# Optimization experiments

Measured on AMD Instinct MI355X. Metric: run time of the kernel, lower is better.

Reference implementation:

```python
import jax, jax.numpy as jnp
import numpy as np

HEADS = 16
DIM_HEAD = 64


def setup_inputs() -> dict:
    key = jax.random.key(0)
    ks = jax.random.split(key, 5)
    b, n, dim = 4, 2048, 1024
    return {
        "x": jax.random.normal(ks[0], (b, n, dim), dtype=jnp.float32),
        "Wq": jax.random.normal(ks[1], (dim, HEADS * DIM_HEAD), dtype=jnp.float32) * (dim ** -0.5),
        "Wkv": jax.random.normal(ks[2], (dim, DIM_HEAD), dtype=jnp.float32) * (dim ** -0.5),
        "null_kv": jax.random.normal(ks[3], (DIM_HEAD,), dtype=jnp.float32),
        "Wout": jax.random.normal(ks[4], (HEADS * DIM_HEAD, dim), dtype=jnp.float32) * ((HEADS * DIM_HEAD) ** -0.5),
    }


def reference(x, Wq, Wkv, null_kv, Wout):
    b, n, dim = x.shape
    scale = DIM_HEAD ** -0.5
    # q: [b, h, n, d], pre-scaled
    q = (x @ Wq).reshape(b, n, HEADS, DIM_HEAD).transpose(0, 2, 1, 3) * scale
    # shared single-head kv: [b, n, d], prepend null token -> [b, n+1, d]
    kv = x @ Wkv
    kv = jnp.concatenate([jnp.broadcast_to(null_kv, (b, 1, DIM_HEAD)), kv], axis=1)
    # sim: [b, h, n, n+1]
    sim = jnp.einsum('bhid,bjd->bhij', q, kv)
    mask_value = -jnp.finfo(sim.dtype).max
    # causal: query i may attend kv cols 0..i+1 (null at col 0)
    i, j = sim.shape[-2], sim.shape[-1]
    causal_mask = jnp.triu(jnp.ones((i, j), dtype=bool), k=j - i + 1)
    sim = jnp.where(causal_mask, mask_value, sim)
    attn = jax.nn.softmax(sim.astype(jnp.float32), axis=-1)
    out = jnp.einsum('bhij,bjd->bhid', attn, kv.astype(jnp.float32))
    out = out.transpose(0, 2, 1, 3).reshape(b, n, HEADS * DIM_HEAD)
    return out @ Wout
```

## Files before the change

### kernel.cpp

```cpp
#include <hip/hip_runtime.h>
#include <hip/hip_bf16.h>

#define HEADS  16
#define DHEAD  64
#define BATCH  4
#define SEQ    2048
#define DIM    1024
#define KVROWS 2112
#define CSHIFT 24.0f

typedef __hip_bfloat16 bf16;
typedef __attribute__((ext_vector_type(8))) short s8v;
typedef __attribute__((ext_vector_type(4))) short s4v;
typedef __attribute__((ext_vector_type(4))) float f4v;

__device__ __forceinline__ void gl_lds16(const void* g, void* l) {
  __builtin_amdgcn_global_load_lds(
      (const __attribute__((address_space(1))) unsigned int*)g,
      (__attribute__((address_space(3))) unsigned int*)l, 16, 0, 0);
}

__global__ void convert_kernel(const float* __restrict__ in, bf16* __restrict__ out) {
  const size_t i = ((size_t)blockIdx.x * 256 + threadIdx.x) * 8;
  const float4 a = *(const float4*)&in[i];
  const float4 b = *(const float4*)&in[i + 4];
  bf16 v[8] = {__float2bfloat16(a.x), __float2bfloat16(a.y),
               __float2bfloat16(a.z), __float2bfloat16(a.w),
               __float2bfloat16(b.x), __float2bfloat16(b.y),
               __float2bfloat16(b.z), __float2bfloat16(b.w)};
  *(s8v*)&out[i] = *(s8v*)v;
}

__global__ void transpose_kernel(const float* __restrict__ in, bf16* __restrict__ out,
                                 int R, int C) {
  __shared__ bf16 tile[32][33];
  const int c0 = blockIdx.x * 32, r0 = blockIdx.y * 32;
  const int tx = threadIdx.x, ty = threadIdx.y;
#pragma unroll
  for (int i = 0; i < 32; i += 8)
    tile[ty + i][tx] = __float2bfloat16(in[(size_t)(r0 + ty + i) * C + c0 + tx]);
  __syncthreads();
#pragma unroll
  for (int i = 0; i < 32; i += 8)
    out[(size_t)(c0 + ty + i) * R + r0 + tx] = tile[tx][ty + i];
}

template <typename OT>
__global__ __launch_bounds__(256) void gemm_async_kernel(
    const bf16* __restrict__ A, const bf16* __restrict__ BT,
    OT* __restrict__ C, int K, int c_ld, float alpha) {
  __shared__ bf16 As[128 * 32];
  __shared__ bf16 Bs[128 * 32];
  const int m0 = blockIdx.x * 128, n0 = blockIdx.y * 128;
  const int t = threadIdx.x;
  const int w = t >> 6, l = t & 63, lr = l & 15, lq = l >> 4;
  const int wm = (w & 1) * 64, wn = (w >> 1) * 64;
  f4v acc[4][4] = {};

  const int rowl = l >> 2;
  const int cl = ((l & 3) ^ ((l >> 3) & 3)) * 8;
  const bf16* gA0 = A  + (size_t)(m0 + 32 * w + rowl) * K + cl;
  const bf16* gA1 = A  + (size_t)(m0 + 32 * w + 16 + rowl) * K + cl;
  const bf16* gB0 = BT + (size_t)(n0 + 32 * w + rowl) * K + cl;
  const bf16* gB1 = BT + (size_t)(n0 + 32 * w + 16 + rowl) * K + cl;
  bf16* lA0 = As + (2 * w) * 512;
  bf16* lA1 = As + (2 * w + 1) * 512;
  bf16* lB0 = Bs + (2 * w) * 512;
  bf16* lB1 = Bs + (2 * w + 1) * 512;

  const int sw = lq ^ ((lr >> 1) & 3);
  const s8v* As16 = (const s8v*)As;
  const s8v* Bs16 = (const s8v*)Bs;

  for (int k0 = 0; k0 < K; k0 += 32) {
    __syncthreads();
    gl_lds16(gA0 + k0, lA0);
    gl_lds16(gA1 + k0, lA1);
    gl_lds16(gB0 + k0, lB0);
    gl_lds16(gB1 + k0, lB1);
    __syncthreads();
    s8v a[4], b[4];
#pragma unroll
    for (int mt = 0; mt < 4; mt++) a[mt] = As16[(wm + mt * 16 + lr) * 4 + sw];
#pragma unroll
    for (int ct = 0; ct < 4; ct++) b[ct] = Bs16[(wn + ct * 16 + lr) * 4 + sw];
#pragma unroll
    for (int mt = 0; mt < 4; mt++)
#pragma unroll
      for (int ct = 0; ct < 4; ct++)
        acc[mt][ct] = __builtin_amdgcn_mfma_f32_16x16x32_bf16(a[mt], b[ct], acc[mt][ct], 0, 0, 0);
  }
#pragma unroll
  for (int mt = 0; mt < 4; mt++)
#pragma unroll
    for (int ct = 0; ct < 4; ct++)
#pragma unroll
      for (int r = 0; r < 4; r++) {
        const int row = m0 + wm + mt * 16 + lq * 4 + r;
        const int col = n0 + wn + ct * 16 + lr;
        const float v = acc[mt][ct][r] * alpha;
        if constexpr (__is_same(OT, float)) C[(size_t)row * c_ld + col] = v;
        else                                C[(size_t)row * c_ld + col] = __float2bfloat16(v);
      }
}

__global__ __launch_bounds__(256) void gemm_kv_kernel(
    const bf16* __restrict__ A, const bf16* __restrict__ BT,
    bf16* __restrict__ kvbuf, bf16* __restrict__ kvbufT, int K) {
  __shared__ bf16 As[128][32];
  __shared__ bf16 Bs[64][32];
  const int m0 = blockIdx.x * 128;
  const int t = threadIdx.x;
  const int w = t >> 6, l = t & 63, lr = l & 15, lq = l >> 4;
  f4v acc[2][4] = {};
  const int arow = t >> 1, acol = (t & 1) * 16;
  const int brow = t >> 2, bcol = (t & 3) * 8;

  for (int k0 = 0; k0 < K; k0 += 32) {
    __syncthreads();
    *(s8v*)&As[arow][acol]     = *(const s8v*)&A[(size_t)(m0 + arow) * K + k0 + acol];
    *(s8v*)&As[arow][acol + 8] = *(const s8v*)&A[(size_t)(m0 + arow) * K + k0 + acol + 8];
    *(s8v*)&Bs[brow][bcol]     = *(const s8v*)&BT[(size_t)brow * K + k0 + bcol];
    __syncthreads();
    s8v a0 = *(const s8v*)&As[w * 32 + lr][lq * 8];
    s8v a1 = *(const s8v*)&As[w * 32 + 16 + lr][lq * 8];
#pragma unroll
    for (int ct = 0; ct < 4; ct++) {
      s8v bf = *(const s8v*)&Bs[ct * 16 + lr][lq * 8];
      acc[0][ct] = __builtin_amdgcn_mfma_f32_16x16x32_bf16(a0, bf, acc[0][ct], 0, 0, 0);
      acc[1][ct] = __builtin_amdgcn_mfma_f32_16x16x32_bf16(a1, bf, acc[1][ct], 0, 0, 0);
    }
  }
#pragma unroll
  for (int mt = 0; mt < 2; mt++)
#pragma unroll
    for (int ct = 0; ct < 4; ct++)
#pragma unroll
      for (int r = 0; r < 4; r++) {
        const int m = m0 + w * 32 + mt * 16 + lq * 4 + r;
        const int col = ct * 16 + lr;
        const int bb = m >> 11, jj = (m & 2047) + 1;
        const bf16 v = __float2bfloat16(acc[mt][ct][r]);
        kvbuf [(size_t)(bb * KVROWS + jj) * DHEAD + col] = v;
        kvbufT[(size_t)(bb * DHEAD + col) * KVROWS + jj] = v;
      }
}

__global__ void fill_null_tail_kernel(const float* __restrict__ null_kv,
                                      bf16* __restrict__ kvbuf,
                                      bf16* __restrict__ kvbufT) {
  const int idx = blockIdx.x * 256 + threadIdx.x;
  const int d = idx & 63;
  const int s = (idx >> 6) & 63;
  const int b = idx >> 12;
  const int row = (s == 0) ? 0 : 2048 + s;
  const bf16 v = (s == 0) ? __float2bfloat16(null_kv[d]) : __float2bfloat16(0.f);
  kvbuf [(size_t)(b * KVROWS + row) * DHEAD + d] = v;
  kvbufT[(size_t)(b * DHEAD + d) * KVROWS + row] = v;
}

__global__ __launch_bounds__(256) void attn_kernel(
    const bf16* __restrict__ q,
    const bf16* __restrict__ kv,
    const bf16* __restrict__ kvT,
    bf16* __restrict__ o) {
  __shared__ bf16 kvs [64][68];
  __shared__ bf16 kvsT[64][68];
  __shared__ bf16 Ps[4][16][68];
  const int t = threadIdx.x, w = t >> 6, l = t & 63, lr = l & 15, lq = l >> 4;
  const int blk = blockIdx.x;
  const int qt = 31 - (blk >> 5);
  const int rem = blk & 31, hp = rem >> 2, b = rem & 3;
  const int q0 = qt * 64;
  const int iw = q0 + w * 16 + lr;

  const bf16* qbase = q + ((size_t)(b * SEQ) + iw) * DIM + hp * 128;
  s8v qb[2][2];
#pragma unroll
  for (int hh = 0; hh < 2; hh++) {
    qb[hh][0] = *(const s8v*)&qbase[hh * 64 + lq * 8];
    qb[hh][1] = *(const s8v*)&qbase[hh * 64 + 32 + lq * 8];
  }

  f4v oaccT[2][4] = {};
  f4v lacc[2] = {};
  const short onebf = (short)0x3F80;
  const s8v ones = {onebf, onebf, onebf, onebf, onebf, onebf, onebf, onebf};

  const bf16* kvb  = kv  + (size_t)b * KVROWS * DHEAD;
  const bf16* kvTb = kvT + (size_t)b * DHEAD * KVROWS;
  const int jend = q0 + 65;
  const int srow = t >> 2, scol = (t & 3) * 16;

  s8v rkv0 = *(const s8v*)&kvb[(size_t)srow * DHEAD + scol];
  s8v rkv1 = *(const s8v*)&kvb[(size_t)srow * DHEAD + scol + 8];
  s8v rkT0 = *(const s8v*)&kvTb[(size_t)srow * KVROWS + scol];
  s8v rkT1 = *(const s8v*)&kvTb[(size_t)srow * KVROWS + scol + 8];

  for (int j0 = 0; j0 < jend; j0 += 64) {
    __syncthreads();
    *(s8v*)&kvs[srow][scol]      = rkv0;
    *(s8v*)&kvs[srow][scol + 8]  = rkv1;
    *(s8v*)&kvsT[srow][scol]     = rkT0;
    *(s8v*)&kvsT[srow][scol + 8] = rkT1;
    __syncthreads();

    const int jn = min(j0 + 64, KVROWS - 64);
    rkv0 = *(const s8v*)&kvb[(size_t)(jn + srow) * DHEAD + scol];
    rkv1 = *(const s8v*)&kvb[(size_t)(jn + srow) * DHEAD + scol + 8];
    rkT0 = *(const s8v*)&kvTb[(size_t)srow * KVROWS + jn + scol];
    rkT1 = *(const s8v*)&kvTb[(size_t)srow * KVROWS + jn + scol + 8];

    f4v st[2][4];
    __builtin_amdgcn_s_setprio(1);
#pragma unroll
    for (int jt = 0; jt < 4; jt++) {
      s8v a0 = *(const s8v*)&kvs[jt * 16 + lr][lq * 8];
      s8v a1 = *(const s8v*)&kvs[jt * 16 + lr][32 + lq * 8];
#pragma unroll
      for (int hh = 0; hh < 2; hh++) {
        f4v z = {-CSHIFT, -CSHIFT, -CSHIFT, -CSHIFT};
        z = __builtin_amdgcn_mfma_f32_16x16x32_bf16(a0, qb[hh][0], z, 0, 0, 0);
        z = __builtin_amdgcn_mfma_f32_16x16x32_bf16(a1, qb[hh][1], z, 0, 0, 0);
        st[hh][jt] = z;
      }
    }
    __builtin_amdgcn_s_setprio(0);

    const bool diag = (j0 + 62 > q0 + w * 16);
    s8v pb[2][2];
#pragma unroll
    for (int hh = 0; hh < 2; hh++) {
      if (diag) {
#pragma unroll
        for (int jt = 0; jt < 4; jt++)
#pragma unroll
          for (int r = 0; r < 4; r++) {
            const int jg = j0 + jt * 16 + lq * 4 + r;
            if (jg > iw + 1) st[hh][jt][r] = -1e30f;
          }
      }
#pragma unroll
      for (int jt = 0; jt < 4; jt++)
#pragma unroll
        for (int r = 0; r < 4; r++)
          st[hh][jt][r] = exp2f(st[hh][jt][r]);

#pragma unroll
      for (int jt = 0; jt < 4; jt++) {
        s4v pk;
#pragma unroll
        for (int r = 0; r < 4; r++) {
          bf16 h16 = __float2bfloat16(st[hh][jt][r]);
          pk[r] = *(short*)&h16;
        }
        *(s4v*)&Ps[w][lr][jt * 16 + lq * 4] = pk;
      }
      pb[hh][0] = *(const s8v*)&Ps[w][lr][lq * 8];
      pb[hh][1] = *(const s8v*)&Ps[w][lr][32 + lq * 8];
    }

    __builtin_amdgcn_s_setprio(1);
#pragma unroll
    for (int hh = 0; hh < 2; hh++) {
      lacc[hh] = __builtin_amdgcn_mfma_f32_16x16x32_bf16(ones, pb[hh][0], lacc[hh], 0, 0, 0);
      lacc[hh] = __builtin_amdgcn_mfma_f32_16x16x32_bf16(ones, pb[hh][1], lacc[hh], 0, 0, 0);
    }
#pragma unroll
    for (int dt = 0; dt < 4; dt++) {
      s8v a0 = *(const s8v*)&kvsT[dt * 16 + lr][lq * 8];
      s8v a1 = *(const s8v*)&kvsT[dt * 16 + lr][32 + lq * 8];
#pragma unroll
      for (int hh = 0; hh < 2; hh++) {
        oaccT[hh][dt] = __builtin_amdgcn_mfma_f32_16x16x32_bf16(a0, pb[hh][0], oaccT[hh][dt], 0, 0, 0);
        oaccT[hh][dt] = __builtin_amdgcn_mfma_f32_16x16x32_bf16(a1, pb[hh][1], oaccT[hh][dt], 0, 0, 0);
      }
    }
    __builtin_amdgcn_s_setprio(0);
  }

#pragma unroll
  for (int hh = 0; hh < 2; hh++) {
    const float inv = 1.0f / lacc[hh][0];
#pragma unroll
    for (int dt = 0; dt < 4; dt++) {
      s4v pk;
#pragma unroll
      for (int r = 0; r < 4; r++) {
        bf16 h16 = __float2bfloat16(oaccT[hh][dt][r] * inv);
        pk[r] = *(short*)&h16;
      }
      *(s4v*)&Ps[w][lr][dt * 16 + lq * 4] = pk;
    }
    const int orow = l >> 2, od = (l & 3) * 16;
    s8v o0 = *(const s8v*)&Ps[w][orow][od];
    s8v o1 = *(const s8v*)&Ps[w][orow][od + 8];
    bf16* op = o + ((size_t)(b * SEQ) + q0 + w * 16 + orow) * DIM + hp * 128 + hh * 64 + od;
    *(s8v*)&op[0] = o0;
    *(s8v*)&op[8] = o1;
  }
}

extern "C" void kernel_launch(void* const* d_in, const int* in_sizes, int n_in,
                              void* d_out, int out_size, void* d_ws, size_t ws_size,
                              hipStream_t stream) {
  const float* x       = (const float*)d_in[0];
  const float* Wq      = (const float*)d_in[1];
  const float* Wkv     = (const float*)d_in[2];
  const float* null_kv = (const float*)d_in[3];
  const float* Wout    = (const float*)d_in[4];
  float* out = (float*)d_out;

  char* dob = (char*)d_out;
  bf16* q      = (bf16*)dob;
  bf16* kvbufT = (bf16*)(dob + (size_t)16 * 1024 * 1024);
  char* p = (char*)d_ws;
  bf16* att   = (bf16*)p;
  bf16* xb    = (bf16*)(p + (size_t)16 * 1024 * 1024);
  bf16* WoutT = (bf16*)(p + (size_t)32 * 1024 * 1024);
  bf16* kvbuf = (bf16*)(p + (size_t)34 * 1024 * 1024);
  bf16* WqT   = att;
  bf16* WkvT  = att + (size_t)DIM * DIM;

  convert_kernel<<<(BATCH * SEQ * DIM) / (256 * 8), 256, 0, stream>>>(x, xb);

  const dim3 tb(32, 8);
  transpose_kernel<<<dim3(32, 32), tb, 0, stream>>>(Wq,   WqT,   DIM, DIM);
  transpose_kernel<<<dim3(2, 32),  tb, 0, stream>>>(Wkv,  WkvT,  DIM, DHEAD);
  transpose_kernel<<<dim3(32, 32), tb, 0, stream>>>(Wout, WoutT, DIM, DIM);

  gemm_async_kernel<bf16><<<dim3(64, 8), 256, 0, stream>>>(xb, WqT, q, DIM, DIM,
                                                           0.125f * 1.44269504089f);
  gemm_kv_kernel<<<64, 256, 0, stream>>>(xb, WkvT, kvbuf, kvbufT, DIM);
  fill_null_tail_kernel<<<(BATCH * 64 * 64) / 256, 256, 0, stream>>>(null_kv, kvbuf, kvbufT);

  attn_kernel<<<32 * 8 * BATCH, 256, 0, stream>>>(q, kvbuf, kvbufT, att);

  gemm_async_kernel<float><<<dim3(64, 8), 256, 0, stream>>>(att, WoutT, out, DIM, DIM, 1.0f);
}
```

Before: 255.5 us.

## Split long causal attention tiles across two blocks and add combine kernel

Query tiles in the upper half of the sequence now have their KV range split between two blocks, each writing unnormalised bf16 partial outputs and row sums. A new combine kernel adds the two partials and normalises them. This balances the causal workload and raises the block count from 1024 to 1536 to shorten the long tail of the heaviest tiles. The cost is an extra launch, the partial-buffer traffic and the bf16 rounding of unnormalised partials. The setprio hints are also dropped and the PV MFMAs are interleaved per head.

```diff
diff --git a/kernel.cpp b/kernel.cpp
--- a/kernel.cpp
+++ b/kernel.cpp
@@ -163,16 +163,34 @@
     const bf16* __restrict__ q,
     const bf16* __restrict__ kv,
     const bf16* __restrict__ kvT,
-    bf16* __restrict__ o) {
+    bf16* __restrict__ o,
+    bf16* __restrict__ opart,
+    float* __restrict__ lpart) {
   __shared__ bf16 kvs [64][68];
   __shared__ bf16 kvsT[64][68];
   __shared__ bf16 Ps[4][16][68];
   const int t = threadIdx.x, w = t >> 6, l = t & 63, lr = l & 15, lq = l >> 4;
   const int blk = blockIdx.x;
-  const int qt = 31 - (blk >> 5);
-  const int rem = blk & 31, hp = rem >> 2, b = rem & 3;
+  int qt, hp, b, half;
+  bool split;
+  if (blk < 1024) {
+    split = true;
+    qt = 31 - (blk >> 6);
+    const int rem = blk & 63;
+    half = rem >> 5; hp = (rem >> 2) & 7; b = rem & 3;
+  } else {
+    split = false;
+    const int r2 = blk - 1024;
+    qt = 15 - (r2 >> 5);
+    const int rem = r2 & 31;
+    half = 0; hp = rem >> 2; b = rem & 3;
+  }
   const int q0 = qt * 64;
   const int iw = q0 + w * 16 + lr;
+  const int nA    = (qt + 3) >> 1;
+  const int js0   = (split && half) ? nA * 64 : 0;
+  const int jend  = (split && !half) ? nA * 64 : q0 + 65;
+  const int jlast = (jend - 1) & ~63;
 
   const bf16* qbase = q + ((size_t)(b * SEQ) + iw) * DIM + hp * 128;
   s8v qb[2][2];
@@ -189,15 +207,14 @@
 
   const bf16* kvb  = kv  + (size_t)b * KVROWS * DHEAD;
   const bf16* kvTb = kvT + (size_t)b * DHEAD * KVROWS;
-  const int jend = q0 + 65;
   const int srow = t >> 2, scol = (t & 3) * 16;
 
-  s8v rkv0 = *(const s8v*)&kvb[(size_t)srow * DHEAD + scol];
-  s8v rkv1 = *(const s8v*)&kvb[(size_t)srow * DHEAD + scol + 8];
-  s8v rkT0 = *(const s8v*)&kvTb[(size_t)srow * KVROWS + scol];
-  s8v rkT1 = *(const s8v*)&kvTb[(size_t)srow * KVROWS + scol + 8];
-
-  for (int j0 = 0; j0 < jend; j0 += 64) {
+  s8v rkv0 = *(const s8v*)&kvb[(size_t)(js0 + srow) * DHEAD + scol];
+  s8v rkv1 = *(const s8v*)&kvb[(size_t)(js0 + srow) * DHEAD + scol + 8];
+  s8v rkT0 = *(const s8v*)&kvTb[(size_t)srow * KVROWS + js0 + scol];
+  s8v rkT1 = *(const s8v*)&kvTb[(size_t)srow * KVROWS + js0 + scol + 8];
+
+  for (int j0 = js0; j0 < jend; j0 += 64) {
     __syncthreads();
     *(s8v*)&kvs[srow][scol]      = rkv0;
     *(s8v*)&kvs[srow][scol + 8]  = rkv1;
@@ -205,14 +222,13 @@
     *(s8v*)&kvsT[srow][scol + 8] = rkT1;
     __syncthreads();
 
-    const int jn = min(j0 + 64, KVROWS - 64);
+    const int jn = min(j0 + 64, jlast);
     rkv0 = *(const s8v*)&kvb[(size_t)(jn + srow) * DHEAD + scol];
     rkv1 = *(const s8v*)&kvb[(size_t)(jn + srow) * DHEAD + scol + 8];
     rkT0 = *(const s8v*)&kvTb[(size_t)srow * KVROWS + jn + scol];
     rkT1 = *(const s8v*)&kvTb[(size_t)srow * KVROWS + jn + scol + 8];
 
     f4v st[2][4];
-    __builtin_amdgcn_s_setprio(1);
 #pragma unroll
     for (int jt = 0; jt < 4; jt++) {
       s8v a0 = *(const s8v*)&kvs[jt * 16 + lr][lq * 8];
@@ -225,10 +241,8 @@
         st[hh][jt] = z;
       }
     }
-    __builtin_amdgcn_s_setprio(0);
 
     const bool diag = (j0 + 62 > q0 + w * 16);
-    s8v pb[2][2];
 #pragma unroll
     for (int hh = 0; hh < 2; hh++) {
       if (diag) {
@@ -256,38 +270,94 @@
         }
         *(s4v*)&Ps[w][lr][jt * 16 + lq * 4] = pk;
       }
-      pb[hh][0] = *(const s8v*)&Ps[w][lr][lq * 8];
-      pb[hh][1] = *(const s8v*)&Ps[w][lr][32 + lq * 8];
-    }
-
-    __builtin_amdgcn_s_setprio(1);
+      const s8v pb0 = *(const s8v*)&Ps[w][lr][lq * 8];
+      const s8v pb1 = *(const s8v*)&Ps[w][lr][32 + lq * 8];
+
+      lacc[hh] = __builtin_amdgcn_mfma_f32_16x16x32_bf16(ones, pb0, lacc[hh], 0, 0, 0);
+      lacc[hh] = __builtin_amdgcn_mfma_f32_16x16x32_bf16(ones, pb1, lacc[hh], 0, 0, 0);
+
+#pragma unroll
+      for (int dt = 0; dt < 4; dt++) {
+        s8v a0 = *(const s8v*)&kvsT[dt * 16 + lr][lq * 8];
+        s8v a1 = *(const s8v*)&kvsT[dt * 16 + lr][32 + lq * 8];
+        oaccT[hh][dt] = __builtin_amdgcn_mfma_f32_16x16x32_bf16(a0, pb0, oaccT[hh][dt], 0, 0, 0);
+        oaccT[hh][dt] = __builtin_amdgcn_mfma_f32_16x16x32_bf16(a1, pb1, oaccT[hh][dt], 0, 0, 0);
+      }
+    }
+  }
+
+  if (!split) {
 #pragma unroll
     for (int hh = 0; hh < 2; hh++) {
-      lacc[hh] = __builtin_amdgcn_mfma_f32_16x16x32_bf16(ones, pb[hh][0], lacc[hh], 0, 0, 0);
-      lacc[hh] = __builtin_amdgcn_mfma_f32_16x16x32_bf16(ones, pb[hh][1], lacc[hh], 0, 0, 0);
-    }
+      const float inv = 1.0f / lacc[hh][0];
+#pragma unroll
+      for (int dt = 0; dt < 4; dt++) {
+        s4v pk;
+#pragma unroll
+        for (int r = 0; r < 4; r++) {
+          bf16 h16 = __float2bfloat16(oaccT[hh][dt][r] * inv);
+          pk[r] = *(short*)&h16;
+        }
+        *(s4v*)&Ps[w][lr][dt * 16 + lq * 4] = pk;
+      }
+      const int orow = l >> 2, od = (l & 3) * 16;
+      s8v o0 = *(const s8v*)&Ps[w][orow][od];
+      s8v o1 = *(const s8v*)&Ps[w][orow][od + 8];
+      bf16* op = o + ((size_t)(b * SEQ) + q0 + w * 16 + orow) * DIM + hp * 128 + hh * 64 + od;
+      *(s8v*)&op[0] = o0;
+      *(s8v*)&op[8] = o1;
+    }
+  } else {
+    const int comb = ((qt - 16) * 8 + hp) * 4 + b;
+    bf16* ob = opart + ((size_t)(comb * 2 + half)) * 8192;
+#pragma unroll
+    for (int hh = 0; hh < 2; hh++) {
+#pragma unroll
+      for (int dt = 0; dt < 4; dt++) {
+        s4v pk;
+#pragma unroll
+        for (int r = 0; r < 4; r++) {
+          bf16 h16 = __float2bfloat16(oaccT[hh][dt][r]);
+          pk[r] = *(short*)&h16;
+        }
+        *(s4v*)&ob[(size_t)((((w * 2 + hh) * 4 + dt) * 64 + l) * 4)] = pk;
+      }
+      if (lq == 0)
+        lpart[(((size_t)(comb * 2 + half) * 4 + w) * 2 + hh) * 16 + lr] = lacc[hh][0];
+    }
+  }
+}
+
+__global__ __launch_bounds__(256) void combine_kernel(
+    const bf16* __restrict__ opart, const float* __restrict__ lpart,
+    bf16* __restrict__ o) {
+  __shared__ bf16 Ps[4][16][68];
+  const int t = threadIdx.x, w = t >> 6, l = t & 63, lr = l & 15, lq = l >> 4;
+  const int blk = blockIdx.x;
+  const int qs = blk >> 5;
+  const int rem = blk & 31, hp = rem >> 2, b = rem & 3;
+  const int qt = qs + 16, q0 = qt * 64;
+  const int comb = (qs * 8 + hp) * 4 + b;
+  const bf16* oA = opart + (size_t)(comb * 2 + 0) * 8192;
+  const bf16* oB = opart + (size_t)(comb * 2 + 1) * 8192;
+
+#pragma unroll
+  for (int hh = 0; hh < 2; hh++) {
+    const float lA = lpart[(((size_t)(comb * 2 + 0) * 4 + w) * 2 + hh) * 16 + lr];
+    const float lB = lpart[(((size_t)(comb * 2 + 1) * 4 + w) * 2 + hh) * 16 + lr];
+    const float inv = 1.0f / (lA + lB);
 #pragma unroll
     for (int dt = 0; dt < 4; dt++) {
-      s8v a0 = *(const s8v*)&kvsT[dt * 16 + lr][lq * 8];
-      s8v a1 = *(const s8v*)&kvsT[dt * 16 + lr][32 + lq * 8];
-#pragma unroll
-      for (int hh = 0; hh < 2; hh++) {
-        oaccT[hh][dt] = __builtin_amdgcn_mfma_f32_16x16x32_bf16(a0, pb[hh][0], oaccT[hh][dt], 0, 0, 0);
-        oaccT[hh][dt] = __builtin_amdgcn_mfma_f32_16x16x32_bf16(a1, pb[hh][1], oaccT[hh][dt], 0, 0, 0);
-      }
-    }
-    __builtin_amdgcn_s_setprio(0);
-  }
-
-#pragma unroll
-  for (int hh = 0; hh < 2; hh++) {
-    const float inv = 1.0f / lacc[hh][0];
-#pragma unroll
-    for (int dt = 0; dt < 4; dt++) {
+      const size_t off = (size_t)((((w * 2 + hh) * 4 + dt) * 64 + l) * 4);
+      const s4v pa = *(const s4v*)&oA[off];
+      const s4v pc = *(const s4v*)&oB[off];
       s4v pk;
 #pragma unroll
       for (int r = 0; r < 4; r++) {
-        bf16 h16 = __float2bfloat16(oaccT[hh][dt][r] * inv);
+        short sa = pa[r], sc = pc[r];
+        const float va = __bfloat162float(*(bf16*)&sa);
+        const float vc = __bfloat162float(*(bf16*)&sc);
+        bf16 h16 = __float2bfloat16((va + vc) * inv);
         pk[r] = *(short*)&h16;
       }
       *(s4v*)&Ps[w][lr][dt * 16 + lq * 4] = pk;
@@ -314,6 +384,7 @@
   char* dob = (char*)d_out;
   bf16* q      = (bf16*)dob;
   bf16* kvbufT = (bf16*)(dob + (size_t)16 * 1024 * 1024);
+  float* lpart = (float*)(dob + (size_t)18 * 1024 * 1024);
   char* p = (char*)d_ws;
   bf16* att   = (bf16*)p;
   bf16* xb    = (bf16*)(p + (size_t)16 * 1024 * 1024);
@@ -321,6 +392,7 @@
   bf16* kvbuf = (bf16*)(p + (size_t)34 * 1024 * 1024);
   bf16* WqT   = att;
   bf16* WkvT  = att + (size_t)DIM * DIM;
+  bf16* opart = xb;
 
   convert_kernel<<<(BATCH * SEQ * DIM) / (256 * 8), 256, 0, stream>>>(x, xb);
 
@@ -334,7 +406,8 @@
   gemm_kv_kernel<<<64, 256, 0, stream>>>(xb, WkvT, kvbuf, kvbufT, DIM);
   fill_null_tail_kernel<<<(BATCH * 64 * 64) / 256, 256, 0, stream>>>(null_kv, kvbuf, kvbufT);
 
-  attn_kernel<<<32 * 8 * BATCH, 256, 0, stream>>>(q, kvbuf, kvbufT, att);
+  attn_kernel<<<1536, 256, 0, stream>>>(q, kvbuf, kvbufT, att, opart, lpart);
+  combine_kernel<<<512, 256, 0, stream>>>(opart, lpart, att);
 
   gemm_async_kernel<float><<<dim3(64, 8), 256, 0, stream>>>(att, WoutT, out, DIM, DIM, 1.0f);
 }
```

New measurement: 257.7 us. About the same (+0.9%).

## Load K/V fragments directly from global memory, dropping LDS staging and barriers

Applied to the files above, without the earlier changes.

The attention kernel no longer stages each 64-row K and V^T tile through shared memory with register prefetch and two block barriers per iteration. Each wave now reads its MFMA operand fragments straight from global memory, which is L2-cached and shared by the four waves. The s_setprio hints are also removed. This cuts LDS traffic and synchronisation, but every wave issues redundant global loads and loses the software prefetch, so the MFMAs may stall on memory latency.

```diff
diff --git a/kernel.cpp b/kernel.cpp
--- a/kernel.cpp
+++ b/kernel.cpp
@@ -164,8 +164,6 @@
     const bf16* __restrict__ kv,
     const bf16* __restrict__ kvT,
     bf16* __restrict__ o) {
-  __shared__ bf16 kvs [64][68];
-  __shared__ bf16 kvsT[64][68];
   __shared__ bf16 Ps[4][16][68];
   const int t = threadIdx.x, w = t >> 6, l = t & 63, lr = l & 15, lq = l >> 4;
   const int blk = blockIdx.x;
@@ -190,33 +188,14 @@
   const bf16* kvb  = kv  + (size_t)b * KVROWS * DHEAD;
   const bf16* kvTb = kvT + (size_t)b * DHEAD * KVROWS;
   const int jend = q0 + 65;
-  const int srow = t >> 2, scol = (t & 3) * 16;
-
-  s8v rkv0 = *(const s8v*)&kvb[(size_t)srow * DHEAD + scol];
-  s8v rkv1 = *(const s8v*)&kvb[(size_t)srow * DHEAD + scol + 8];
-  s8v rkT0 = *(const s8v*)&kvTb[(size_t)srow * KVROWS + scol];
-  s8v rkT1 = *(const s8v*)&kvTb[(size_t)srow * KVROWS + scol + 8];
 
   for (int j0 = 0; j0 < jend; j0 += 64) {
-    __syncthreads();
-    *(s8v*)&kvs[srow][scol]      = rkv0;
-    *(s8v*)&kvs[srow][scol + 8]  = rkv1;
-    *(s8v*)&kvsT[srow][scol]     = rkT0;
-    *(s8v*)&kvsT[srow][scol + 8] = rkT1;
-    __syncthreads();
-
-    const int jn = min(j0 + 64, KVROWS - 64);
-    rkv0 = *(const s8v*)&kvb[(size_t)(jn + srow) * DHEAD + scol];
-    rkv1 = *(const s8v*)&kvb[(size_t)(jn + srow) * DHEAD + scol + 8];
-    rkT0 = *(const s8v*)&kvTb[(size_t)srow * KVROWS + jn + scol];
-    rkT1 = *(const s8v*)&kvTb[(size_t)srow * KVROWS + jn + scol + 8];
-
     f4v st[2][4];
-    __builtin_amdgcn_s_setprio(1);
 #pragma unroll
     for (int jt = 0; jt < 4; jt++) {
-      s8v a0 = *(const s8v*)&kvs[jt * 16 + lr][lq * 8];
-      s8v a1 = *(const s8v*)&kvs[jt * 16 + lr][32 + lq * 8];
+      const bf16* kr = kvb + (size_t)(j0 + jt * 16 + lr) * DHEAD;
+      const s8v a0 = *(const s8v*)&kr[lq * 8];
+      const s8v a1 = *(const s8v*)&kr[32 + lq * 8];
 #pragma unroll
       for (int hh = 0; hh < 2; hh++) {
         f4v z = {-CSHIFT, -CSHIFT, -CSHIFT, -CSHIFT};
@@ -225,7 +204,6 @@
         st[hh][jt] = z;
       }
     }
-    __builtin_amdgcn_s_setprio(0);
 
     const bool diag = (j0 + 62 > q0 + w * 16);
     s8v pb[2][2];
@@ -258,25 +236,22 @@
       }
       pb[hh][0] = *(const s8v*)&Ps[w][lr][lq * 8];
       pb[hh][1] = *(const s8v*)&Ps[w][lr][32 + lq * 8];
-    }
-
-    __builtin_amdgcn_s_setprio(1);
-#pragma unroll
-    for (int hh = 0; hh < 2; hh++) {
+
       lacc[hh] = __builtin_amdgcn_mfma_f32_16x16x32_bf16(ones, pb[hh][0], lacc[hh], 0, 0, 0);
       lacc[hh] = __builtin_amdgcn_mfma_f32_16x16x32_bf16(ones, pb[hh][1], lacc[hh], 0, 0, 0);
     }
+
 #pragma unroll
     for (int dt = 0; dt < 4; dt++) {
-      s8v a0 = *(const s8v*)&kvsT[dt * 16 + lr][lq * 8];
-      s8v a1 = *(const s8v*)&kvsT[dt * 16 + lr][32 + lq * 8];
+      const bf16* vr = kvTb + (size_t)(dt * 16 + lr) * KVROWS + j0;
+      const s8v a0 = *(const s8v*)&vr[lq * 8];
+      const s8v a1 = *(const s8v*)&vr[32 + lq * 8];
 #pragma unroll
       for (int hh = 0; hh < 2; hh++) {
         oaccT[hh][dt] = __builtin_amdgcn_mfma_f32_16x16x32_bf16(a0, pb[hh][0], oaccT[hh][dt], 0, 0, 0);
         oaccT[hh][dt] = __builtin_amdgcn_mfma_f32_16x16x32_bf16(a1, pb[hh][1], oaccT[hh][dt], 0, 0, 0);
       }
     }
-    __builtin_amdgcn_s_setprio(0);
   }
 
 #pragma unroll
```

Measured after the change: 317.9 us. +24.4%, slower.
